# Kernel optimization log

Measured on AMD Instinct MI355X. Metric: run time of the kernel, lower is better.

## Reference

```python
import jax, jax.numpy as jnp
import numpy as np


def setup_inputs() -> dict:
    key = jax.random.key(0)
    k1, k2, k3, k4 = jax.random.split(key, 4)
    B, T, C, H = 16, 2048, 1024, 128
    x = jax.random.normal(k1, (B, T, C), dtype=jnp.float32)
    # bias-free Dense kernels (stored as [in, out] like keras)
    s = 1.0 / np.sqrt(C)
    Wk = jax.random.normal(k2, (C, H), dtype=jnp.float32) * s
    Wq = jax.random.normal(k3, (C, H), dtype=jnp.float32) * s
    Wv = jax.random.normal(k4, (C, H), dtype=jnp.float32) * s
    return {"x": x, "Wk": Wk, "Wq": Wq, "Wv": Wv}


def reference(x, Wk, Wq, Wv):
    # single-head causal self-attention (dropout inactive at inference)
    B, T, C = x.shape
    H = Wk.shape[-1]
    k = jnp.einsum('btc,ch->bth', x, Wk)   # [B,T,H]
    q = jnp.einsum('btc,ch->bth', x, Wq)
    v = jnp.einsum('btc,ch->bth', x, Wv)
    scale = 1.0 / jnp.sqrt(jnp.float32(H))
    wei = jnp.einsum('bqh,bkh->bqk', q, k) * scale          # [B,T,T]
    causal = jnp.tril(jnp.ones((T, T), dtype=bool))
    wei = jnp.where(causal, wei, -jnp.inf)
    wei = jax.nn.softmax(wei, axis=-1)
    out = jnp.einsum('bqk,bkh->bqh', wei, v)                # [B,T,H]
    return out
```

## Files before the change

kernel.cpp:

```cpp
#include <hip/hip_runtime.h>
#include <hip/hip_bf16.h>

typedef __bf16 bf16x8_t __attribute__((ext_vector_type(8)));
typedef __bf16 bf16x4_t __attribute__((ext_vector_type(4)));
typedef float  f32x4_t  __attribute__((ext_vector_type(4)));

#define MFMA_16x16x32_BF16(A, B, C) __builtin_amdgcn_mfma_f32_16x16x32_bf16((A), (B), (C), 0, 0, 0)

static constexpr int B_ = 16;
static constexpr int T_ = 2048;
static constexpr int C_ = 1024;
static constexpr int H_ = 128;
static constexpr long M_ = (long)B_ * T_;

__device__ __forceinline__ void gload_lds16(const void* g, void* l)
{
    __builtin_amdgcn_global_load_lds(
        (const __attribute__((address_space(1))) void*)g,
        (__attribute__((address_space(3))) void*)l, 16, 0, 0);
}

__global__ __launch_bounds__(256) void wt_kernel(
    const float* __restrict__ Wq, const float* __restrict__ Wk,
    const float* __restrict__ Wv, __bf16* __restrict__ WB)
{
    const int pair = blockIdx.x * 4 + (threadIdx.x >> 6);
    const int lane = threadIdx.x & 63;
    const int m16  = lane & 15;
    const int quad = lane >> 4;
    const int nt   = pair >> 5;
    const int t    = pair & 31;
    const int z    = nt >> 3;
    const int h    = (nt & 7) * 16 + m16;
    const float* __restrict__ W = (z == 0) ? Wq : (z == 1) ? Wk : Wv;

    bf16x8_t v;
    #pragma unroll
    for (int e = 0; e < 8; ++e)
        v[e] = (__bf16)W[(t * 32 + quad * 8 + e) * H_ + h];
    *(bf16x8_t*)&WB[((long)pair * 64 + lane) * 8] = v;
}

__global__ __launch_bounds__(256, 4) void proj_kernel(
    const float*  __restrict__ x,
    const __bf16* __restrict__ WB,
    __bf16* __restrict__ qo,
    __bf16* __restrict__ ko,
    __bf16* __restrict__ vo)
{
    __shared__ float XS[2][32 * 32];

    const int tid  = threadIdx.x;
    const int w    = tid >> 6;
    const int lane = tid & 63;
    const int m16  = lane & 15;
    const int quad = lane >> 4;

    const long r0 = (long)blockIdx.x * 32;

    const int xl_row = lane >> 3;
    const int xl_u   = (lane & 7) ^ xl_row;

    const __bf16* __restrict__ wp = WB + ((long)(w * 6) * 32 + 0) * 512 + lane * 8;

    f32x4_t acc[2][6];
    #pragma unroll
    for (int hh = 0; hh < 2; ++hh)
        #pragma unroll
        for (int j = 0; j < 6; ++j) acc[hh][j] = f32x4_t{0, 0, 0, 0};

#define XSTAGE(T, BUF)                                                       \
    gload_lds16(&x[(r0 + w * 8 + xl_row) * C_ + (T) * 32 + xl_u * 4],        \
                &XS[BUF][w * 8 * 32]);

    XSTAGE(0, 0);
    __syncthreads();

    const int asw = m16 & 7;

    for (int t = 0; t < 32; ++t) {
        const int cur = t & 1;
        if (t < 31) XSTAGE(t + 1, cur ^ 1);

        bf16x8_t b[6];
        #pragma unroll
        for (int j = 0; j < 6; ++j)
            b[j] = *(const bf16x8_t*)(wp + ((long)j * 32 + t) * 512);

        bf16x8_t a[2];
        #pragma unroll
        for (int hh = 0; hh < 2; ++hh) {
            const int row = hh * 16 + m16;
            f32x4_t lo = *(const f32x4_t*)&XS[cur][row * 32 + (((quad * 2 + 0) ^ asw) << 2)];
            f32x4_t hi = *(const f32x4_t*)&XS[cur][row * 32 + (((quad * 2 + 1) ^ asw) << 2)];
            #pragma unroll
            for (int jj = 0; jj < 4; ++jj) {
                a[hh][jj]     = (__bf16)lo[jj];
                a[hh][4 + jj] = (__bf16)hi[jj];
            }
        }

        #pragma unroll
        for (int j = 0; j < 6; ++j)
            #pragma unroll
            for (int hh = 0; hh < 2; ++hh)
                acc[hh][j] = MFMA_16x16x32_BF16(a[hh], b[j], acc[hh][j]);

        __syncthreads();
    }
#undef XSTAGE

    #pragma unroll
    for (int hh = 0; hh < 2; ++hh) {
        const long rbase = r0 + hh * 16 + quad * 4;
        #pragma unroll
        for (int j = 0; j < 6; ++j) {
            const int nt = w * 6 + j;
            const int z  = nt >> 3;
            const int h  = (nt & 7) * 16 + m16;
            if (z < 2) {
                __bf16* __restrict__ o = z ? ko : qo;
                #pragma unroll
                for (int r = 0; r < 4; ++r)
                    o[(rbase + r) * H_ + h] = (__bf16)acc[hh][j][r];
            } else {
                long bb = rbase >> 11, tt = rbase & 2047;
                bf16x4_t pk;
                #pragma unroll
                for (int r = 0; r < 4; ++r) pk[r] = (__bf16)acc[hh][j][r];
                *(bf16x4_t*)&vo[bb * (H_ * (long)T_) + h * (long)T_ + tt] = pk;
            }
        }
    }
}

__global__ __launch_bounds__(256) void attn_kernel(
    const __bf16* __restrict__ q,
    const __bf16* __restrict__ k,
    const __bf16* __restrict__ vT,
    float* __restrict__ out)
{
    __shared__ __bf16 KS[64 * 136];
    __shared__ __bf16 VS[128 * 72];
    __shared__ __bf16 PS[4][16 * 72];

    const int L   = blockIdx.x;
    const int b   = L & 15;
    const int Lh  = L >> 4;
    const int qb  = (Lh < 16) ? (31 - Lh) : (Lh - 16);

    const int tid  = threadIdx.x;
    const int w    = tid >> 6;
    const int lane = tid & 63;
    const int m16  = lane & 15;
    const int quad = lane >> 4;
    const int koff = quad * 8;

    const __bf16* __restrict__ qp = q  + (long)b * T_ * H_;
    const __bf16* __restrict__ kp = k  + (long)b * T_ * H_;
    const __bf16* __restrict__ vp = vT + (long)b * H_ * T_;

    const int q0w = qb * 64 + w * 16;
    const int qg  = q0w + m16;

    bf16x8_t qfr[4];
    #pragma unroll
    for (int s = 0; s < 4; ++s)
        qfr[s] = *(const bf16x8_t*)&qp[(q0w + m16) * H_ + s * 32 + koff];

    f32x4_t acc[8];
    #pragma unroll
    for (int i = 0; i < 8; ++i) acc[i] = f32x4_t{0, 0, 0, 0};
    float mrun = -1e30f, lrun = 0.f;

    __bf16* Pb = &PS[w][0];
    const float SC = 0.08838834764831845f;
    const int kend = qb * 64 + 64;

    const int krow = tid >> 4, kc16 = tid & 15;
    const int vrow = tid >> 3, vc8  = tid & 7;

    for (int tk0 = 0; tk0 < kend; tk0 += 64) {
        __syncthreads();
        #pragma unroll
        for (int ch = 0; ch < 4; ++ch) {
            int r = krow + ch * 16;
            *(bf16x8_t*)&KS[r * 136 + kc16 * 8] =
                *(const bf16x8_t*)&kp[(tk0 + r) * H_ + kc16 * 8];
        }
        #pragma unroll
        for (int ch = 0; ch < 4; ++ch) {
            int hh = vrow + ch * 32;
            *(bf16x8_t*)&VS[hh * 72 + vc8 * 8] =
                *(const bf16x8_t*)&vp[hh * (long)T_ + tk0 + vc8 * 8];
        }
        __syncthreads();

        f32x4_t st[4];
        #pragma unroll
        for (int kt = 0; kt < 4; ++kt) {
            f32x4_t s = f32x4_t{0, 0, 0, 0};
            #pragma unroll
            for (int sI = 0; sI < 4; ++sI) {
                bf16x8_t kf = *(const bf16x8_t*)&KS[(kt * 16 + m16) * 136 + sI * 32 + koff];
                s = MFMA_16x16x32_BF16(kf, qfr[sI], s);
            }
            st[kt] = s;
        }

        float vv[4][4];
        if (tk0 + 63 <= q0w) {
            #pragma unroll
            for (int kt = 0; kt < 4; ++kt)
                #pragma unroll
                for (int r = 0; r < 4; ++r)
                    vv[kt][r] = st[kt][r] * SC;
        } else {
            #pragma unroll
            for (int kt = 0; kt < 4; ++kt)
                #pragma unroll
                for (int r = 0; r < 4; ++r) {
                    int kg = tk0 + kt * 16 + quad * 4 + r;
                    vv[kt][r] = (kg <= qg) ? st[kt][r] * SC : -1e30f;
                }
        }

        float mloc = -1e30f;
        #pragma unroll
        for (int kt = 0; kt < 4; ++kt)
            #pragma unroll
            for (int r = 0; r < 4; ++r)
                mloc = fmaxf(mloc, vv[kt][r]);
        mloc = fmaxf(mloc, __shfl_xor(mloc, 16, 64));
        mloc = fmaxf(mloc, __shfl_xor(mloc, 32, 64));

        float mnew = fmaxf(mrun, mloc);
        float al   = __expf(mrun - mnew);
        float psum = 0.f;
        #pragma unroll
        for (int kt = 0; kt < 4; ++kt) {
            bf16x4_t pk;
            #pragma unroll
            for (int r = 0; r < 4; ++r) {
                float p = __expf(vv[kt][r] - mnew);
                psum += p;
                pk[r] = (__bf16)p;
            }
            *(bf16x4_t*)&Pb[m16 * 72 + kt * 16 + quad * 4] = pk;
        }
        psum += __shfl_xor(psum, 16, 64);
        psum += __shfl_xor(psum, 32, 64);
        mrun = mnew;
        lrun = lrun * al + psum;

        #pragma unroll
        for (int i = 0; i < 8; ++i)
            #pragma unroll
            for (int r = 0; r < 4; ++r)
                acc[i][r] *= al;

        #pragma unroll
        for (int half = 0; half < 2; ++half) {
            bf16x8_t pa = *(const bf16x8_t*)&Pb[m16 * 72 + half * 32 + koff];
            #pragma unroll
            for (int i = 0; i < 8; ++i) {
                bf16x8_t vf = *(const bf16x8_t*)&VS[(i * 16 + m16) * 72 + half * 32 + koff];
                acc[i] = MFMA_16x16x32_BF16(vf, pa, acc[i]);
            }
        }
    }

    float* __restrict__ ob = out + (long)b * T_ * H_;
    const float inv = 1.f / lrun;
    #pragma unroll
    for (int i = 0; i < 8; ++i) {
        f32x4_t o;
        #pragma unroll
        for (int r = 0; r < 4; ++r) o[r] = acc[i][r] * inv;
        *(f32x4_t*)&ob[(q0w + m16) * H_ + i * 16 + quad * 4] = o;
    }
}

extern "C" void kernel_launch(void* const* d_in, const int* in_sizes, int n_in,
                              void* d_out, int out_size, void* d_ws, size_t ws_size,
                              hipStream_t stream)
{
    const float* x  = (const float*)d_in[0];
    const float* Wk = (const float*)d_in[1];
    const float* Wq = (const float*)d_in[2];
    const float* Wv = (const float*)d_in[3];

    __bf16* qws = (__bf16*)d_ws;
    __bf16* kws = qws + M_ * H_;
    __bf16* vws = kws + M_ * H_;
    __bf16* WB  = vws + (long)B_ * H_ * T_;
    float*  out = (float*)d_out;

    wt_kernel  <<<dim3(192), 256, 0, stream>>>(Wq, Wk, Wv, WB);
    proj_kernel<<<dim3((int)(M_ / 32)), 256, 0, stream>>>(x, WB, qws, kws, vws);
    attn_kernel<<<dim3(512), 256, 0, stream>>>(qws, kws, vws, out);
}
```

Baseline: 290.0 us.

## Triple-buffer x staging and double-buffer weight registers in projection kernel

```diff
diff --git a/kernel.cpp b/kernel.cpp
--- a/kernel.cpp
+++ b/kernel.cpp
@@ -48,7 +48,7 @@
     __bf16* __restrict__ ko,
     __bf16* __restrict__ vo)
 {
-    __shared__ float XS[2][32 * 32];
+    __shared__ float XS[3][32 * 32];
 
     const int tid  = threadIdx.x;
     const int w    = tid >> 6;
@@ -61,7 +61,7 @@
     const int xl_row = lane >> 3;
     const int xl_u   = (lane & 7) ^ xl_row;
 
-    const __bf16* __restrict__ wp = WB + ((long)(w * 6) * 32 + 0) * 512 + lane * 8;
+    const __bf16* __restrict__ wp = WB + (long)(w * 6) * 32 * 512 + lane * 8;
 
     f32x4_t acc[2][6];
     #pragma unroll
@@ -73,26 +73,36 @@
     gload_lds16(&x[(r0 + w * 8 + xl_row) * C_ + (T) * 32 + xl_u * 4],        \
                 &XS[BUF][w * 8 * 32]);
 
+    bf16x8_t bb[2][6];
+
     XSTAGE(0, 0);
-    __syncthreads();
+    XSTAGE(1, 1);
+    #pragma unroll
+    for (int j = 0; j < 6; ++j)
+        bb[0][j] = *(const bf16x8_t*)(wp + (long)j * 32 * 512);
+    asm volatile("s_waitcnt vmcnt(7)" ::: "memory");
+    __builtin_amdgcn_sched_barrier(0);
+    __builtin_amdgcn_s_barrier();
+    __builtin_amdgcn_sched_barrier(0);
 
     const int asw = m16 & 7;
 
+    #pragma unroll
     for (int t = 0; t < 32; ++t) {
-        const int cur = t & 1;
-        if (t < 31) XSTAGE(t + 1, cur ^ 1);
-
-        bf16x8_t b[6];
-        #pragma unroll
-        for (int j = 0; j < 6; ++j)
-            b[j] = *(const bf16x8_t*)(wp + ((long)j * 32 + t) * 512);
+        if (t + 2 < 32) XSTAGE(t + 2, (t + 2) % 3);
+        if (t + 1 < 32) {
+            #pragma unroll
+            for (int j = 0; j < 6; ++j)
+                bb[(t + 1) & 1][j] =
+                    *(const bf16x8_t*)(wp + ((long)j * 32 + (t + 1)) * 512);
+        }
 
         bf16x8_t a[2];
         #pragma unroll
         for (int hh = 0; hh < 2; ++hh) {
             const int row = hh * 16 + m16;
-            f32x4_t lo = *(const f32x4_t*)&XS[cur][row * 32 + (((quad * 2 + 0) ^ asw) << 2)];
-            f32x4_t hi = *(const f32x4_t*)&XS[cur][row * 32 + (((quad * 2 + 1) ^ asw) << 2)];
+            f32x4_t lo = *(const f32x4_t*)&XS[t % 3][row * 32 + (((quad * 2 + 0) ^ asw) << 2)];
+            f32x4_t hi = *(const f32x4_t*)&XS[t % 3][row * 32 + (((quad * 2 + 1) ^ asw) << 2)];
             #pragma unroll
             for (int jj = 0; jj < 4; ++jj) {
                 a[hh][jj]     = (__bf16)lo[jj];
@@ -104,9 +114,15 @@
         for (int j = 0; j < 6; ++j)
             #pragma unroll
             for (int hh = 0; hh < 2; ++hh)
-                acc[hh][j] = MFMA_16x16x32_BF16(a[hh], b[j], acc[hh][j]);
-
-        __syncthreads();
+                acc[hh][j] = MFMA_16x16x32_BF16(a[hh], bb[t & 1][j], acc[hh][j]);
+
+        if (t < 31) {
+            __builtin_amdgcn_sched_barrier(0);
+            if (t + 2 < 32) asm volatile("s_waitcnt vmcnt(7)" ::: "memory");
+            else            asm volatile("s_waitcnt vmcnt(6)" ::: "memory");
+            __builtin_amdgcn_s_barrier();
+            __builtin_amdgcn_sched_barrier(0);
+        }
     }
 #undef XSTAGE
 
@@ -124,11 +140,11 @@
                 for (int r = 0; r < 4; ++r)
                     o[(rbase + r) * H_ + h] = (__bf16)acc[hh][j][r];
             } else {
-                long bb = rbase >> 11, tt = rbase & 2047;
+                long bb2 = rbase >> 11, tt = rbase & 2047;
                 bf16x4_t pk;
                 #pragma unroll
                 for (int r = 0; r < 4; ++r) pk[r] = (__bf16)acc[hh][j][r];
-                *(bf16x4_t*)&vo[bb * (H_ * (long)T_) + h * (long)T_ + tt] = pk;
+                *(bf16x4_t*)&vo[bb2 * (H_ * (long)T_) + h * (long)T_ + tt] = pk;
             }
         }
     }
```

Measured after the change: 290.2 us. About the same (+0.1%).
